# Kernel tuning notes

Measured on AMD Instinct MI355X. Metric: run time of the kernel, lower is better.

The kernel has to match this reference:

```python
import jax, jax.numpy as jnp
import numpy as np

N = 50000          # nodes
E = 400000         # edges (avg degree 8)
F_IN = 144         # n_node_features + n_graph_features = 128 + 16
F_OUT = 128        # n_node_features
DIMS = [(F_IN, 256), (256, 512), (512, 256), (256, F_OUT)]


def setup_inputs() -> dict:
    key = jax.random.key(0)
    ks = jax.random.split(key, 16)
    lin = lambda k, fi, fo: (jax.random.normal(k, (fo, fi), jnp.float32) / np.sqrt(fi).astype(np.float32))
    inp = {}
    inp["x"] = jax.random.normal(ks[0], (N, F_IN), jnp.float32)
    inp["edge_index"] = jax.random.randint(ks[1], (2, E), 0, N)
    inp["edge_attr"] = jax.random.uniform(ks[2], (E,), jnp.float32)
    for i, (fi, fo) in enumerate(DIMS):
        inp[f"W_rel{i+1}"] = lin(ks[3 + 3 * i], fi, fo)
        inp[f"b_rel{i+1}"] = jnp.zeros((fo,), jnp.float32)
        inp[f"W_root{i+1}"] = lin(ks[4 + 3 * i], fi, fo)
    inp["gn_w"] = jnp.ones((256,), jnp.float32)
    inp["gn_b"] = jnp.zeros((256,), jnp.float32)
    inp["gn_ms"] = jnp.ones((256,), jnp.float32)
    return inp


def graph_conv(x, src, dst, w, W_rel, b_rel, W_root):
    # PyG GraphConv (aggr='add'): out = lin_rel(sum_{j->i} w_e * x_j) + lin_root(x)
    agg = jax.ops.segment_sum(x[src] * w[:, None], dst, num_segments=x.shape[0])
    return agg @ W_rel.T + b_rel + x @ W_root.T


def graph_norm(x, w, b, ms, eps=1e-5):
    # PyG GraphNorm (single graph): centered by learnable mean_scale, var of centered
    mu = x.mean(axis=0, keepdims=True)
    c = x - ms * mu
    var = (c * c).mean(axis=0, keepdims=True)
    return c / jnp.sqrt(var + eps) * w + b


def reference(x, edge_index, edge_attr,
              W_rel1, b_rel1, W_root1,
              W_rel2, b_rel2, W_root2,
              W_rel3, b_rel3, W_root3,
              W_rel4, b_rel4, W_root4,
              gn_w, gn_b, gn_ms):
    src, dst = edge_index[0], edge_index[1]
    h = jax.nn.relu(graph_conv(x, src, dst, edge_attr, W_rel1, b_rel1, W_root1))
    h = jax.nn.relu(graph_conv(h, src, dst, edge_attr, W_rel2, b_rel2, W_root2))
    h = graph_conv(h, src, dst, edge_attr, W_rel3, b_rel3, W_root3)
    h = jax.nn.relu(graph_norm(h, gn_w, gn_b, gn_ms))
    return graph_conv(h, src, dst, edge_attr, W_rel4, b_rel4, W_root4)
```

## Files before the change

kernel.cpp:

```cpp
#include <hip/hip_runtime.h>

#define F_IN 144
typedef __attribute__((ext_vector_type(8))) short short8v;
typedef __attribute__((ext_vector_type(8))) unsigned short ushort8v;
typedef __attribute__((ext_vector_type(4))) float f32x4;
typedef unsigned short u16;

__device__ __forceinline__ u16 bf16rn(float x) {
    union { float f; unsigned u; } a; a.f = x;
    return (u16)((a.u + 0x7FFFu + ((a.u >> 16) & 1u)) >> 16);
}
__device__ __forceinline__ float bf16tof(u16 h) {
    union { float f; unsigned u; } a; a.u = ((unsigned)h) << 16;
    return a.f;
}
__device__ __forceinline__ void gload_lds16(const u16* g, u16* s) {
    __builtin_amdgcn_global_load_lds(
        (const __attribute__((address_space(1))) void*)g,
        (__attribute__((address_space(3))) void*)s, 16, 0, 0);
}

__global__ void zero_i32(int* __restrict__ p, int n) {
    int i = blockIdx.x * blockDim.x + threadIdx.x;
    if (i < n) p[i] = 0;
}
__global__ void zero_f32(float* __restrict__ p, int n) {
    int i = blockIdx.x * blockDim.x + threadIdx.x;
    if (i < n) p[i] = 0.f;
}
__global__ void conv_hl(const float* __restrict__ src, u16* __restrict__ dh,
                        u16* __restrict__ dl, int n) {
    int i = blockIdx.x * 256 + threadIdx.x;
    if (i < n) {
        float v = src[i];
        u16 h = bf16rn(v);
        dh[i] = h;
        dl[i] = bf16rn(v - bf16tof(h));
    }
}
__global__ void conv_bf(const float* __restrict__ src, u16* __restrict__ d, int n) {
    int i = blockIdx.x * 256 + threadIdx.x;
    if (i < n) d[i] = bf16rn(src[i]);
}

__global__ void count_edges(const int* __restrict__ dst, int* __restrict__ counts, int E) {
    int e = blockIdx.x * blockDim.x + threadIdx.x;
    if (e < E) atomicAdd(&counts[dst[e]], 1);
}

#define SCB 2048
__global__ __launch_bounds__(256) void scan_partial(const int* __restrict__ counts,
                                                    int* __restrict__ rowptr,
                                                    int* __restrict__ bsum, int N) {
    __shared__ int ls[256];
    int t = threadIdx.x;
    int base = blockIdx.x * SCB + t * 8;
    int v[8]; int s = 0;
#pragma unroll
    for (int j = 0; j < 8; ++j) {
        int i = base + j;
        v[j] = (i < N) ? counts[i] : 0;
        s += v[j];
    }
    ls[t] = s;
    __syncthreads();
    for (int off = 1; off < 256; off <<= 1) {
        int x = (t >= off) ? ls[t - off] : 0;
        __syncthreads();
        ls[t] += x;
        __syncthreads();
    }
    int run = (t == 0) ? 0 : ls[t - 1];
#pragma unroll
    for (int j = 0; j < 8; ++j) {
        int i = base + j;
        if (i < N) rowptr[i] = run;
        run += v[j];
    }
    if (t == 255) bsum[blockIdx.x] = ls[255];
}

__global__ __launch_bounds__(256) void scan_tops(const int* __restrict__ bsum,
                                                 int* __restrict__ boff, int nb) {
    __shared__ int ls[256];
    int t = threadIdx.x;
    ls[t] = (t < nb) ? bsum[t] : 0;
    __syncthreads();
    for (int off = 1; off < 256; off <<= 1) {
        int x = (t >= off) ? ls[t - off] : 0;
        __syncthreads();
        ls[t] += x;
        __syncthreads();
    }
    boff[t] = (t == 0) ? 0 : ls[t - 1];
}

__global__ void scan_add(int* __restrict__ rowptr, int* __restrict__ fillhead,
                         const int* __restrict__ boff, int N, int E) {
    int i = blockIdx.x * 256 + threadIdx.x;
    if (i < N) {
        int r = rowptr[i] + boff[i >> 11];
        rowptr[i] = r;
        fillhead[i] = r;
    }
    if (i == N) rowptr[N] = E;
}

__global__ void fill_edges(const int* __restrict__ src, const int* __restrict__ dst,
                           const float* __restrict__ ea, int* __restrict__ fillhead,
                           int* __restrict__ col, float* __restrict__ wv, int E) {
    int e = blockIdx.x * blockDim.x + threadIdx.x;
    if (e < E) {
        int d = dst[e];
        int pos = atomicAdd(&fillhead[d], 1);
        col[pos] = src[e];
        wv[pos]  = ea[e];
    }
}

template<int NC, int NPW, int MODE>
__global__ __launch_bounds__(256) void aggregate_sp(
    const u16* __restrict__ S, int SS,
    const int* __restrict__ rowptr, const int* __restrict__ col,
    const float* __restrict__ wv,
    const u16* __restrict__ R,
    u16* __restrict__ D, float* __restrict__ Df, int FD, int N)
{
    int wav  = (int)((blockIdx.x * 256 + threadIdx.x) >> 6);
    int lane = threadIdx.x & 63;
    int sub  = lane / NC;
    int cl   = lane % NC;
    int wid  = wav * NPW + sub;
    if (sub >= NPW || wid >= N) return;
    float acc0[8] = {}, acc1[8] = {}, acc2[8] = {}, acc3[8] = {};
    int beg = rowptr[wid], end = rowptr[wid + 1];
    int e = beg;
    for (; e + 4 <= end; e += 4) {
        float w0 = wv[e], w1 = wv[e + 1], w2 = wv[e + 2], w3 = wv[e + 3];
        int   c0 = col[e], c1 = col[e + 1], c2 = col[e + 2], c3 = col[e + 3];
        ushort8v v0 = *(const ushort8v*)&S[(size_t)c0 * SS + (cl << 3)];
        ushort8v v1 = *(const ushort8v*)&S[(size_t)c1 * SS + (cl << 3)];
        ushort8v v2 = *(const ushort8v*)&S[(size_t)c2 * SS + (cl << 3)];
        ushort8v v3 = *(const ushort8v*)&S[(size_t)c3 * SS + (cl << 3)];
#pragma unroll
        for (int r = 0; r < 8; ++r) {
            acc0[r] = fmaf(w0, bf16tof(v0[r]), acc0[r]);
            acc1[r] = fmaf(w1, bf16tof(v1[r]), acc1[r]);
            acc2[r] = fmaf(w2, bf16tof(v2[r]), acc2[r]);
            acc3[r] = fmaf(w3, bf16tof(v3[r]), acc3[r]);
        }
    }
    for (; e < end; ++e) {
        float w0 = wv[e];
        ushort8v v0 = *(const ushort8v*)&S[(size_t)col[e] * SS + (cl << 3)];
#pragma unroll
        for (int r = 0; r < 8; ++r) acc0[r] = fmaf(w0, bf16tof(v0[r]), acc0[r]);
    }
#pragma unroll
    for (int r = 0; r < 8; ++r) acc0[r] += (acc1[r] + acc2[r]) + acc3[r];
    if (MODE >= 1) {
        ushort8v v = *(const ushort8v*)&R[(size_t)wid * SS + (cl << 3)];
#pragma unroll
        for (int r = 0; r < 8; ++r) acc0[r] += bf16tof(v[r]);
    }
    if (MODE == 2) {
        float* o = &Df[(size_t)wid * FD + (cl << 3)];
        *(float4*)o       = make_float4(acc0[0], acc0[1], acc0[2], acc0[3]);
        *(float4*)(o + 4) = make_float4(acc0[4], acc0[5], acc0[6], acc0[7]);
    } else {
        ushort8v o;
#pragma unroll
        for (int r = 0; r < 8; ++r) o[r] = bf16rn(acc0[r]);
        *(ushort8v*)&D[(size_t)wid * FD + (cl << 3)] = o;
    }
}

#define GBM 128
#define GBN 128

template<bool DUALK, int BT>
__global__ __launch_bounds__(256) void gemm7(
    const u16* __restrict__ A1, const u16* __restrict__ A2,
    const u16* __restrict__ B1h, const u16* __restrict__ B1l,
    const u16* __restrict__ B2h, const u16* __restrict__ B2l,
    const float* __restrict__ biasA, const float* __restrict__ biasB,
    u16* __restrict__ Ch,
    int M, int K1, int NR1, int ldc, int doRelu)
{
    constexpr int NP  = 1 + BT;
    constexpr int NCH = 2 * NP;
    constexpr int BUF = NP * 4096;
    __shared__ u16 lds[3 * BUF];

    const int tid = threadIdx.x;
    const int l = tid & 63, w = tid >> 6;
    const int wm = w >> 1, wn = w & 1;
    const int lane15 = l & 15, slot = l >> 4;

    const int nwg = gridDim.x * gridDim.y;
    const int bid = blockIdx.y * gridDim.x + blockIdx.x;
    const int q = nwg >> 3, r8 = nwg & 7;
    const int xcd = bid & 7, v = bid >> 3;
    const int sw = (xcd < r8) ? xcd * (q + 1) + v : r8 * (q + 1) + (xcd - r8) * q + v;
    const int row0 = (sw / gridDim.x) * GBM;
    const int col0 = (sw % gridDim.x) * GBN;

    const int KK = DUALK ? 2 * K1 : K1;
    const int nsteps = KK / 32;

    const u16* q1[NCH]; const u16* q2[NCH]; int lim[NCH]; int dstoff[NCH];
#pragma unroll
    for (int i = 0; i < NCH; ++i) {
        int idx0  = i * 256 + (tid & ~63);
        int p     = idx0 >> 9;
        int cbase = idx0 & 511;
        int c  = cbase + l;
        int rw = c >> 2, ch = c & 3;
        int cpk = (ch ^ ((rw >> 1) & 3)) << 3;
        lim[i]    = K1 - cpk;
        dstoff[i] = (p << 12) + (cbase << 3);
        const u16 *b1, *b2; int g;
        if (p == 0) {
            b1 = A1; b2 = A2 - K1;
            g = min(row0 + rw, M - 1);
        } else {
            const u16* h1 = (p == 1) ? B1h : B1l;
            const u16* h2 = (p == 1) ? B2h : B2l;
            if (DUALK) { b1 = h1; b2 = h2 - K1; g = col0 + rw; }
            else {
                bool sec = (col0 >= NR1);
                b1 = sec ? h2 : h1; b2 = b1;
                g = col0 + rw - (sec ? NR1 : 0);
            }
        }
        q1[i] = b1 + g * K1 + cpk;
        q2[i] = b2 + g * K1 + cpk;
    }

    auto stage = [&](u16* base, int kk0) {
#pragma unroll
        for (int i = 0; i < NCH; ++i) {
            const u16* s = (DUALK && kk0 >= lim[i]) ? q2[i] : q1[i];
            gload_lds16(s + kk0, base + dstoff[i]);
        }
    };

    f32x4 acc[4][4] = {};

    stage(lds, 0);
    if (nsteps > 1) {
        stage(lds + BUF, 32);
        asm volatile("s_waitcnt vmcnt(%0)" :: "n"(NCH) : "memory");
    } else {
        asm volatile("s_waitcnt vmcnt(0)" ::: "memory");
    }
    __builtin_amdgcn_s_barrier();
    __builtin_amdgcn_sched_barrier(0);

    int ro = 0, so = 2 * BUF;
    for (int step = 0; step < nsteps; ++step) {
        const u16* cb = lds + ro;
        short8v av[4], bh[4], bl[4];
#pragma unroll
        for (int bi = 0; bi < 4; ++bi) {
            int r = wm * 64 + bi * 16 + lane15;
            int j = slot ^ ((r >> 1) & 3);
            av[bi] = *(const short8v*)&cb[r * 32 + j * 8];
        }
#pragma unroll
        for (int bj = 0; bj < 4; ++bj) {
            int c = wn * 64 + bj * 16 + lane15;
            int j = slot ^ ((c >> 1) & 3);
            bh[bj] = *(const short8v*)&cb[4096 + c * 32 + j * 8];
            if (BT == 2) bl[bj] = *(const short8v*)&cb[8192 + c * 32 + j * 8];
        }
        if (step + 2 < nsteps) stage(lds + so, (step + 2) * 32);
#pragma unroll
        for (int bj = 0; bj < 4; ++bj)
#pragma unroll
            for (int bi = 0; bi < 4; ++bi) {
                acc[bi][bj] = __builtin_amdgcn_mfma_f32_16x16x32_bf16(av[bi], bh[bj], acc[bi][bj], 0, 0, 0);
                if (BT == 2)
                    acc[bi][bj] = __builtin_amdgcn_mfma_f32_16x16x32_bf16(av[bi], bl[bj], acc[bi][bj], 0, 0, 0);
            }
        if (step + 1 < nsteps) {
            if (step + 2 < nsteps)
                asm volatile("s_waitcnt vmcnt(%0)" :: "n"(NCH) : "memory");
            else
                asm volatile("s_waitcnt vmcnt(0)" ::: "memory");
            __builtin_amdgcn_s_barrier();
            __builtin_amdgcn_sched_barrier(0);
        }
        ro += BUF; if (ro == 3 * BUF) ro = 0;
        so += BUF; if (so == 3 * BUF) so = 0;
    }

    __syncthreads();
    u16* ct = lds;
#pragma unroll
    for (int bj = 0; bj < 4; ++bj) {
        int cc = wn * 64 + bj * 16 + lane15;
        int gc = col0 + cc;
        float bv = (gc < NR1) ? (biasA ? biasA[gc] : 0.f)
                              : (biasB ? biasB[gc - NR1] : 0.f);
#pragma unroll
        for (int bi = 0; bi < 4; ++bi) {
            int rb = wm * 64 + bi * 16 + slot * 4;
#pragma unroll
            for (int qq = 0; qq < 4; ++qq) {
                float o = acc[bi][bj][qq] + bv;
                if (doRelu) o = fmaxf(o, 0.f);
                ct[(rb + qq) * 132 + cc] = bf16rn(o);
            }
        }
    }
    __syncthreads();
#pragma unroll
    for (int it = 0; it < 8; ++it) {
        int row = it * 16 + (tid >> 4);
        int c16 = (tid & 15) * 8;
        int gr = row0 + row;
        if (gr < M) {
            ushort8v vv = *(const ushort8v*)&ct[row * 132 + c16];
            *(ushort8v*)&Ch[(size_t)gr * ldc + col0 + c16] = vv;
        }
    }
}

__global__ __launch_bounds__(256) void colstats2(const u16* __restrict__ H,
                                                 float* __restrict__ sums,
                                                 float* __restrict__ sqs, int N) {
    __shared__ float lsum[8][256];
    __shared__ float lsq[8][256];
    int t  = threadIdx.x;
    int g  = t >> 5;
    int cl = t & 31;
    float s[8] = {}, q[8] = {};
    for (int row = blockIdx.x * 8 + g; row < N; row += gridDim.x * 8) {
        ushort8v v = *(const ushort8v*)&H[(size_t)row * 256 + (cl << 3)];
#pragma unroll
        for (int r = 0; r < 8; ++r) {
            float f = bf16tof(v[r]);
            s[r] += f;
            q[r] = fmaf(f, f, q[r]);
        }
    }
#pragma unroll
    for (int r = 0; r < 8; ++r) {
        lsum[g][(cl << 3) + r] = s[r];
        lsq[g][(cl << 3) + r]  = q[r];
    }
    __syncthreads();
    float ts = 0.f, tq = 0.f;
#pragma unroll
    for (int gg = 0; gg < 8; ++gg) { ts += lsum[gg][t]; tq += lsq[gg][t]; }
    atomicAdd(&sums[t], ts);
    atomicAdd(&sqs[t], tq);
}

__global__ void norm_prep(const float* __restrict__ sums, const float* __restrict__ sqs,
                          const float* __restrict__ gw, const float* __restrict__ gb,
                          const float* __restrict__ gms, float* __restrict__ scaleF,
                          float* __restrict__ shiftF, float invN) {
    int f = threadIdx.x;
    float mu  = sums[f] * invN;
    float ex2 = sqs[f] * invN;
    float a   = gms[f] * mu;
    float var = ex2 - 2.f * a * mu + a * a;
    float inv = rsqrtf(var + 1e-5f);
    float sc  = gw[f] * inv;
    scaleF[f] = sc;
    shiftF[f] = gb[f] - a * sc;
}

__global__ __launch_bounds__(256) void norm_apply_sp(
    u16* __restrict__ H, const float* __restrict__ scaleF,
    const float* __restrict__ shiftF, int n8) {
    int i = blockIdx.x * 256 + threadIdx.x;
    if (i >= n8) return;
    int f0 = (i & 31) << 3;
    ushort8v h = *(const ushort8v*)&H[(size_t)i * 8];
    ushort8v o;
#pragma unroll
    for (int r = 0; r < 8; ++r) {
        float v = fmaxf(fmaf(bf16tof(h[r]), scaleF[f0 + r], shiftF[f0 + r]), 0.f);
        o[r] = bf16rn(v);
    }
    *(ushort8v*)&H[(size_t)i * 8] = o;
}

extern "C" void kernel_launch(void* const* d_in, const int* in_sizes, int n_in,
                              void* d_out, int out_size, void* d_ws, size_t ws_size,
                              hipStream_t stream) {
    const float* x   = (const float*)d_in[0];
    const int*   ei  = (const int*)d_in[1];
    const float* ea  = (const float*)d_in[2];
    const float* Wr1 = (const float*)d_in[3];
    const float* b1  = (const float*)d_in[4];
    const float* Wo1 = (const float*)d_in[5];
    const float* Wr2 = (const float*)d_in[6];
    const float* b2  = (const float*)d_in[7];
    const float* Wo2 = (const float*)d_in[8];
    const float* Wr3 = (const float*)d_in[9];
    const float* b3  = (const float*)d_in[10];
    const float* Wo3 = (const float*)d_in[11];
    const float* Wr4 = (const float*)d_in[12];
    const float* b4  = (const float*)d_in[13];
    const float* Wo4 = (const float*)d_in[14];
    const float* gw  = (const float*)d_in[15];
    const float* gb  = (const float*)d_in[16];
    const float* gms = (const float*)d_in[17];

    const int Nn = in_sizes[0] / F_IN;
    const int E  = in_sizes[1] / 2;
    const int* src = ei;
    const int* dst = ei + E;

    char* wp = (char*)d_ws;
    auto alloc = [&](size_t bytes) -> void* {
        void* p = (void*)wp;
        wp += (bytes + 255) & ~(size_t)255;
        return p;
    };
    int*   counts   = (int*)alloc((size_t)Nn * 4);
    int*   rowptr   = (int*)alloc((size_t)(Nn + 1) * 4);
    int*   fillhead = (int*)alloc((size_t)Nn * 4);
    int*   col      = (int*)alloc((size_t)E * 4);
    float* wv       = (float*)alloc((size_t)E * 4);
    float* stats    = (float*)alloc(1024 * 4);
    float* sums = stats, *sqs = stats + 256, *scaleF = stats + 512, *shiftF = stats + 768;
    int*   bsum     = (int*)alloc(256 * 4);
    int*   boff     = (int*)alloc(256 * 4);
    u16* wr1 = (u16*)alloc(2u * 256 * 144);
    u16* wo1 = (u16*)alloc(2u * 256 * 144);
    u16* wr2 = (u16*)alloc(2u * 512 * 256);
    u16* wo2 = (u16*)alloc(2u * 512 * 256);
    u16* wr3 = (u16*)alloc(2u * 256 * 512);
    u16* wo3 = (u16*)alloc(2u * 256 * 512);
    u16* wr4h = (u16*)alloc(2u * 128 * 256); u16* wr4l = (u16*)alloc(2u * 128 * 256);
    u16* wo4h = (u16*)alloc(2u * 128 * 256); u16* wo4l = (u16*)alloc(2u * 128 * 256);

    u16* big = (u16*)alloc((size_t)Nn * 1168 * 2);
    const size_t NS = (size_t)Nn;
    u16* Xb  = big;
    u16* AG  = big + NS * 144;
    u16* H1  = big + NS * 400;
    u16* H2  = big + NS * 656;
    u16* Y3  = big;
    u16* H3  = big + NS * 656;
    u16* Y4  = big;

    const int TB = 256;
    int nbScan = (Nn + SCB - 1) / SCB;
    zero_i32<<<(Nn + TB - 1) / TB, TB, 0, stream>>>(counts, Nn);
    count_edges<<<(E + TB - 1) / TB, TB, 0, stream>>>(dst, counts, E);
    scan_partial<<<nbScan, TB, 0, stream>>>(counts, rowptr, bsum, Nn);
    scan_tops<<<1, TB, 0, stream>>>(bsum, boff, nbScan);
    scan_add<<<(Nn + 1 + TB - 1) / TB, TB, 0, stream>>>(rowptr, fillhead, boff, Nn, E);
    fill_edges<<<(E + TB - 1) / TB, TB, 0, stream>>>(src, dst, ea, fillhead, col, wv, E);

    int nx = Nn * F_IN;
    conv_bf<<<(nx + 255) / 256, 256, 0, stream>>>(x, Xb, nx);
    struct BC { const float* s; u16* d; int n; } bc[6] = {
        {Wr1, wr1, 256 * 144}, {Wo1, wo1, 256 * 144},
        {Wr2, wr2, 512 * 256}, {Wo2, wo2, 512 * 256},
        {Wr3, wr3, 256 * 512}, {Wo3, wo3, 256 * 512}};
    for (int i = 0; i < 6; ++i)
        conv_bf<<<(bc[i].n + 255) / 256, 256, 0, stream>>>(bc[i].s, bc[i].d, bc[i].n);
    conv_hl<<<(128 * 256 + 255) / 256, 256, 0, stream>>>(Wr4, wr4h, wr4l, 128 * 256);
    conv_hl<<<(128 * 256 + 255) / 256, 256, 0, stream>>>(Wo4, wo4h, wo4l, 128 * 256);

    int mB = (Nn + GBM - 1) / GBM;
    int g3 = (((Nn + 2) / 3) + 3) / 4;
    int g2 = (((Nn + 1) / 2) + 3) / 4;
    int g4 = (((Nn + 3) / 4) + 3) / 4;

    aggregate_sp<18, 3, 0><<<g3, TB, 0, stream>>>(Xb, 144, rowptr, col, wv,
                                                  nullptr, AG, nullptr, 144, Nn);
    gemm7<true, 1><<<dim3(2, mB), 256, 0, stream>>>(AG, Xb, wr1, nullptr, wo1, nullptr,
                                                    b1, nullptr, H1,
                                                    Nn, 144, 256, 256, 1);
    aggregate_sp<32, 2, 0><<<g2, TB, 0, stream>>>(H1, 256, rowptr, col, wv,
                                                  nullptr, AG, nullptr, 256, Nn);
    gemm7<true, 1><<<dim3(4, mB), 256, 0, stream>>>(AG, H1, wr2, nullptr, wo2, nullptr,
                                                    b2, nullptr, H2,
                                                    Nn, 256, 512, 512, 1);
    gemm7<false, 1><<<dim3(4, mB), 256, 0, stream>>>(H2, H2, wr3, nullptr, wo3, nullptr,
                                                     nullptr, b3, Y3,
                                                     Nn, 512, 256, 512, 0);
    aggregate_sp<32, 2, 1><<<g2, TB, 0, stream>>>(Y3, 512, rowptr, col, wv,
                                                  Y3 + 256, H3, nullptr, 256, Nn);
    zero_f32<<<2, TB, 0, stream>>>(stats, 512);
    colstats2<<<800, TB, 0, stream>>>(H3, sums, sqs, Nn);
    norm_prep<<<1, 256, 0, stream>>>(sums, sqs, gw, gb, gms, scaleF, shiftF, 1.0f / Nn);
    norm_apply_sp<<<(Nn * 32 + TB - 1) / TB, TB, 0, stream>>>(H3, scaleF, shiftF, Nn * 32);
    gemm7<false, 2><<<dim3(2, mB), 256, 0, stream>>>(H3, H3, wr4h, wr4l, wo4h, wo4l,
                                                     nullptr, b4, Y4,
                                                     Nn, 256, 128, 256, 0);
    aggregate_sp<16, 4, 2><<<g4, TB, 0, stream>>>(Y4, 256, rowptr, col, wv,
                                                  Y4 + 128, nullptr, (float*)d_out, 128, Nn);
}
```

Baseline: 377.7 us.

## Add 128x256-tile bf16 GEMM kernel for the first three GraphConv layers

Introduces gemm8, a GEMM with 128x256 output tiles instead of 128x128. Each wave holds a 4x8 grid of MFMA accumulators, and the kernel uses a triple-buffered LDS pipeline with a swizzled layout and an XCD-aware block remap. It replaces gemm7 for layers 1-3 and halves the number of column blocks, so each A tile is loaded from global memory fewer times. In exchange it uses more accumulator registers and LDS per workgroup, which can lower occupancy, and with 50000 rows the grid has fewer workgroups to spread across CUs.

```diff
diff --git a/kernel.cpp b/kernel.cpp
--- a/kernel.cpp
+++ b/kernel.cpp
@@ -175,6 +175,146 @@
     }
 }
 
+template<bool DUALK>
+__global__ __launch_bounds__(256) void gemm8(
+    const u16* __restrict__ A1, const u16* __restrict__ A2,
+    const u16* __restrict__ B1, const u16* __restrict__ B2,
+    const float* __restrict__ biasA, const float* __restrict__ biasB,
+    u16* __restrict__ Ch,
+    int M, int K1, int NR1, int ldc, int doRelu)
+{
+    constexpr int NCH = 6;
+    constexpr int BUF = 12288;
+    __shared__ u16 lds[3 * BUF];
+
+    const int tid = threadIdx.x;
+    const int l = tid & 63, w = tid >> 6;
+    const int wm = w >> 1, wn = w & 1;
+    const int lane15 = l & 15, slot = l >> 4;
+
+    const int nwg = gridDim.x * gridDim.y;
+    const int bid = blockIdx.y * gridDim.x + blockIdx.x;
+    const int q = nwg >> 3, r8 = nwg & 7;
+    const int xcd = bid & 7, v = bid >> 3;
+    const int sw = (xcd < r8) ? xcd * (q + 1) + v : r8 * (q + 1) + (xcd - r8) * q + v;
+    const int row0 = (sw / gridDim.x) * 128;
+    const int col0 = (sw % gridDim.x) * 256;
+
+    const int KK = DUALK ? 2 * K1 : K1;
+    const int nsteps = KK / 32;
+
+    const u16* q1[NCH]; const u16* q2[NCH]; int lim[NCH]; int dstoff[NCH];
+#pragma unroll
+    for (int i = 0; i < NCH; ++i) {
+        int c = i * 256 + tid;
+        bool isA = (c < 512);
+        int cp = isA ? c : (c - 512);
+        int rw = cp >> 2, ch = cp & 3;
+        int cpk = (ch ^ ((rw >> 1) & 3)) << 3;
+        lim[i]    = K1 - cpk;
+        dstoff[i] = (isA ? 0 : 4096) + (cp << 3);
+        const u16 *b1, *b2; int g;
+        if (isA) {
+            b1 = A1; b2 = A2 - K1;
+            g = min(row0 + rw, M - 1);
+        } else {
+            if (DUALK) { b1 = B1; b2 = B2 - K1; g = col0 + rw; }
+            else {
+                bool sec = (col0 >= NR1);
+                b1 = sec ? B2 : B1; b2 = b1;
+                g = col0 + rw - (sec ? NR1 : 0);
+            }
+        }
+        q1[i] = b1 + g * K1 + cpk;
+        q2[i] = b2 + g * K1 + cpk;
+    }
+
+    auto stage = [&](u16* base, int kk0) {
+#pragma unroll
+        for (int i = 0; i < NCH; ++i) {
+            const u16* s = (DUALK && kk0 >= lim[i]) ? q2[i] : q1[i];
+            gload_lds16(s + kk0, base + dstoff[i]);
+        }
+    };
+
+    f32x4 acc[4][8] = {};
+
+    stage(lds, 0);
+    if (nsteps > 1) {
+        stage(lds + BUF, 32);
+        asm volatile("s_waitcnt vmcnt(%0)" :: "n"(NCH) : "memory");
+    } else {
+        asm volatile("s_waitcnt vmcnt(0)" ::: "memory");
+    }
+    __builtin_amdgcn_s_barrier();
+    __builtin_amdgcn_sched_barrier(0);
+
+    int ro = 0, so = 2 * BUF;
+    for (int step = 0; step < nsteps; ++step) {
+        const u16* cb = lds + ro;
+        short8v av[4], bh[8];
+#pragma unroll
+        for (int bi = 0; bi < 4; ++bi) {
+            int r = wm * 64 + bi * 16 + lane15;
+            int j = slot ^ ((r >> 1) & 3);
+            av[bi] = *(const short8v*)&cb[r * 32 + j * 8];
+        }
+#pragma unroll
+        for (int bj = 0; bj < 8; ++bj) {
+            int c = wn * 128 + bj * 16 + lane15;
+            int j = slot ^ ((c >> 1) & 3);
+            bh[bj] = *(const short8v*)&cb[4096 + c * 32 + j * 8];
+        }
+        if (step + 2 < nsteps) stage(lds + so, (step + 2) * 32);
+#pragma unroll
+        for (int bj = 0; bj < 8; ++bj)
+#pragma unroll
+            for (int bi = 0; bi < 4; ++bi)
+                acc[bi][bj] = __builtin_amdgcn_mfma_f32_16x16x32_bf16(av[bi], bh[bj], acc[bi][bj], 0, 0, 0);
+        if (step + 1 < nsteps) {
+            if (step + 2 < nsteps)
+                asm volatile("s_waitcnt vmcnt(%0)" :: "n"(NCH) : "memory");
+            else
+                asm volatile("s_waitcnt vmcnt(0)" ::: "memory");
+            __builtin_amdgcn_s_barrier();
+            __builtin_amdgcn_sched_barrier(0);
+        }
+        ro += BUF; if (ro == 3 * BUF) ro = 0;
+        so += BUF; if (so == 3 * BUF) so = 0;
+    }
+
+    __syncthreads();
+    u16* ct = lds;
+#pragma unroll
+    for (int bj = 0; bj < 8; ++bj) {
+        int cc = wn * 128 + bj * 16 + lane15;
+        int gc = col0 + cc;
+        float bv = (gc < NR1) ? (biasA ? biasA[gc] : 0.f)
+                              : (biasB ? biasB[gc - NR1] : 0.f);
+#pragma unroll
+        for (int bi = 0; bi < 4; ++bi) {
+            int rb = wm * 64 + bi * 16 + slot * 4;
+#pragma unroll
+            for (int qq = 0; qq < 4; ++qq) {
+                float o = acc[bi][bj][qq] + bv;
+                if (doRelu) o = fmaxf(o, 0.f);
+                ct[(rb + qq) * 264 + cc] = bf16rn(o);
+            }
+        }
+    }
+    __syncthreads();
+#pragma unroll
+    for (int it = 0; it < 16; ++it) {
+        int row = it * 8 + (tid >> 5);
+        int c16 = (tid & 31) * 8;
+        int gr = row0 + row;
+        if (gr < M) {
+            ushort8v vv = *(const ushort8v*)&ct[row * 264 + c16];
+            *(ushort8v*)&Ch[(size_t)gr * ldc + col0 + c16] = vv;
+        }
+    }
+}
+
 #define GBM 128
 #define GBN 128
 
@@ -470,24 +610,24 @@
     conv_hl<<<(128 * 256 + 255) / 256, 256, 0, stream>>>(Wr4, wr4h, wr4l, 128 * 256);
     conv_hl<<<(128 * 256 + 255) / 256, 256, 0, stream>>>(Wo4, wo4h, wo4l, 128 * 256);
 
-    int mB = (Nn + GBM - 1) / GBM;
+    int mB = (Nn + 127) / 128;
     int g3 = (((Nn + 2) / 3) + 3) / 4;
     int g2 = (((Nn + 1) / 2) + 3) / 4;
     int g4 = (((Nn + 3) / 4) + 3) / 4;
 
     aggregate_sp<18, 3, 0><<<g3, TB, 0, stream>>>(Xb, 144, rowptr, col, wv,
                                                   nullptr, AG, nullptr, 144, Nn);
-    gemm7<true, 1><<<dim3(2, mB), 256, 0, stream>>>(AG, Xb, wr1, nullptr, wo1, nullptr,
-                                                    b1, nullptr, H1,
-                                                    Nn, 144, 256, 256, 1);
+    gemm8<true><<<dim3(1, mB), 256, 0, stream>>>(AG, Xb, wr1, wo1,
+                                                 b1, nullptr, H1,
+                                                 Nn, 144, 256, 256, 1);
     aggregate_sp<32, 2, 0><<<g2, TB, 0, stream>>>(H1, 256, rowptr, col, wv,
                                                   nullptr, AG, nullptr, 256, Nn);
-    gemm7<true, 1><<<dim3(4, mB), 256, 0, stream>>>(AG, H1, wr2, nullptr, wo2, nullptr,
-                                                    b2, nullptr, H2,
-                                                    Nn, 256, 512, 512, 1);
-    gemm7<false, 1><<<dim3(4, mB), 256, 0, stream>>>(H2, H2, wr3, nullptr, wo3, nullptr,
-                                                     nullptr, b3, Y3,
-                                                     Nn, 512, 256, 512, 0);
+    gemm8<true><<<dim3(2, mB), 256, 0, stream>>>(AG, H1, wr2, wo2,
+                                                 b2, nullptr, H2,
+                                                 Nn, 256, 512, 512, 1);
+    gemm8<false><<<dim3(2, mB), 256, 0, stream>>>(H2, H2, wr3, wo3,
+                                                  nullptr, b3, Y3,
+                                                  Nn, 512, 256, 512, 0);
     aggregate_sp<32, 2, 1><<<g2, TB, 0, stream>>>(Y3, 512, rowptr, col, wv,
                                                   Y3 + 256, H3, nullptr, 256, Nn);
     zero_f32<<<2, TB, 0, stream>>>(stats, 512);
```

New measurement: 425.2 us. +12.6%, slower.
